# Performance work log

Hardware: AMD Instinct MI355X
Metric: run time of the kernel (lower is better)

The kernel has to match this reference:

```python
import jax, jax.numpy as jnp
import numpy as np

N_HEAD = 8
HIDDENS = 512
NEG_INF = -1e9


def setup_inputs() -> dict:
    key = jax.random.key(0)
    ks = jax.random.split(key, 10)
    B, L, KVP, QP, H, W = 8, 1024, 512, 512, 32, 32
    s = 0.02  # init scale
    return {
        "v": jax.random.normal(ks[0], (B, L, KVP), jnp.float32),
        "k": jax.random.normal(ks[1], (B, L, KVP), jnp.float32),
        "q": jax.random.normal(ks[2], (B, QP, H, W), jnp.float32),
        "mask": jax.random.randint(ks[3], (B, 1, 1, L), 0, 2) > 0,
        "Wv": jax.random.normal(ks[4], (HIDDENS, KVP), jnp.float32) * s,
        "bv": jnp.zeros((HIDDENS,), jnp.float32),
        "Wk": jax.random.normal(ks[5], (HIDDENS, KVP), jnp.float32) * s,
        "bk": jnp.zeros((HIDDENS,), jnp.float32),
        "Wq": jax.random.normal(ks[6], (HIDDENS, QP), jnp.float32) * s,
        "bq": jnp.zeros((HIDDENS,), jnp.float32),
        "Wm": jax.random.normal(ks[7], (512, HIDDENS), jnp.float32) * s,
        "bm": jnp.zeros((512,), jnp.float32),
    }


def reference(v, k, q, mask, Wv, bv, Wk, bk, Wq, bq, Wm, bm):
    B, _, H, W = q.shape
    nh, dh = N_HEAD, HIDDENS // N_HEAD
    # k/v linear projections -> [B, nh, L, dh]
    vh = (v @ Wv.T + bv).reshape(B, -1, nh, dh).transpose(0, 2, 1, 3)
    kh = (k @ Wk.T + bk).reshape(B, -1, nh, dh).transpose(0, 2, 1, 3)
    # q 1x1 conv projection -> [B, hiddens, H, W] -> [B, nh, HW, dh]
    qp = jnp.einsum('bchw,oc->bohw', q, Wq) + bq[None, :, None, None]
    qh = qp.reshape(B, nh, dh, H * W).transpose(0, 1, 3, 2)
    # attention: scores fully materialized [B, nh, HW, L]
    scores = jnp.einsum('bnqd,bnkd->bnqk', qh, kh) / jnp.sqrt(jnp.float32(dh))
    scores = jnp.where(mask, NEG_INF, scores)
    att = jax.nn.softmax(scores, axis=-1)  # dropout omitted (eval mode)
    out = jnp.einsum('bnqk,bnkd->bnqd', att, vh)
    # [B, nh, HW, dh] -> [B, hiddens, H, W]
    out = out.transpose(0, 1, 3, 2).reshape(B, HIDDENS, H, W)
    out = jnp.einsum('bchw,oc->bohw', out, Wm) + bm[None, :, None, None]
    return jax.nn.relu(out)
```

## Files before the change

kernel.cpp:

```cpp
#include <hip/hip_runtime.h>

typedef __attribute__((ext_vector_type(8))) __bf16 bf16x8;
typedef __attribute__((ext_vector_type(4))) float  f32x4;

#define SCALE_Q 0.1803368801111204f

__device__ __forceinline__ unsigned short f2bf(float f) {
    unsigned int u = __builtin_bit_cast(unsigned int, f);
    u += 0x7fffu + ((u >> 16) & 1u);
    return (unsigned short)(u >> 16);
}
__device__ __forceinline__ unsigned int pack2(float a, float b) {
    return (unsigned int)f2bf(a) | ((unsigned int)f2bf(b) << 16);
}

__device__ __forceinline__ int idxW(int row, int ch) {
    return row * 512 + (((ch & ~7) | ((ch ^ row) & 7)) << 3);
}
__device__ __forceinline__ int swz8(int row, int chunk) {
    return row * 64 + ((chunk ^ (row & 7)) << 3);
}
__device__ __forceinline__ bf16x8 fragld(const unsigned short* lds, int row, int kk, int lane) {
    return *(const bf16x8*)(lds + swz8(row, kk * 4 + (lane >> 4)));
}

__global__ __launch_bounds__(256) void ck_w(const float* __restrict__ Wv, const float* __restrict__ Wk,
                                            const float* __restrict__ Wq, const float* __restrict__ Wm,
                                            unsigned short* __restrict__ Wp) {
    int tid = threadIdx.x, lane = tid & 63;
    int gw = blockIdx.x * 4 + (tid >> 6);
    int w = gw >> 9, rem = gw & 511;
    int nb = rem >> 4, kb = rem & 15;
    const float* src = (w == 0) ? Wv : (w == 1) ? Wk : (w == 2) ? Wq : Wm;
    const float* gp = src + (size_t)(nb * 16 + (lane & 15)) * 512 + kb * 32 + (lane >> 4) * 8;
    float4 v0 = *(const float4*)gp, v1 = *(const float4*)(gp + 4);
    uint4 o;
    o.x = pack2(v0.x, v0.y); o.y = pack2(v0.z, v0.w);
    o.z = pack2(v1.x, v1.y); o.w = pack2(v1.z, v1.w);
    *(uint4*)(Wp + ((size_t)w << 18) + ((size_t)((nb * 16 + kb) * 64 + lane)) * 8) = o;
}

__global__ __launch_bounds__(256, 2) void g_proj(const float* __restrict__ kin,
                                                 const float* __restrict__ vin,
                                                 const float* __restrict__ qin,
                                                 const unsigned short* __restrict__ Wp,
                                                 const float* __restrict__ bk,
                                                 const float* __restrict__ bv,
                                                 const float* __restrict__ bq,
                                                 unsigned short* __restrict__ kh,
                                                 unsigned short* __restrict__ vh,
                                                 unsigned short* __restrict__ qh) {
    __shared__ alignas(16) unsigned short As[64 * 512];
    int tid = threadIdx.x, lane = tid & 63, wv = tid >> 6;
    int pid = blockIdx.x;
    int srcSel = (pid < 128) ? 0 : (pid < 256) ? 1 : 2;

    if (srcSel < 2) {
        int panel = (srcSel == 0) ? pid : pid - 128;
        const float* src = ((srcSel == 0) ? kin : vin) + (size_t)panel * 64 * 512;
#pragma unroll
        for (int it = 0; it < 16; ++it) {
            int id = it * 256 + tid, row = id >> 6, ch = id & 63;
            const float* gp = src + (size_t)row * 512 + ch * 8;
            float4 a0 = *(const float4*)gp, a1 = *(const float4*)(gp + 4);
            uint4 w;
            w.x = pack2(a0.x, a0.y); w.y = pack2(a0.z, a0.w);
            w.z = pack2(a1.x, a1.y); w.w = pack2(a1.z, a1.w);
            *(uint4*)(&As[idxW(row, ch)]) = w;
        }
    } else {
        int qi = pid - 256, b = qi >> 4, pp = qi & 15;
        const float* src = qin + (size_t)b * 512 * 1024 + pp * 64;
#pragma unroll
        for (int cc = 0; cc < 8; ++cc) {
            int c0 = cc * 64 + (tid >> 4) * 4;
            int pl = (tid & 15) * 4;
            float rr[4][4];
#pragma unroll
            for (int i = 0; i < 4; ++i) {
                float4 t4 = *(const float4*)(src + (size_t)(c0 + i) * 1024 + pl);
                rr[i][0] = t4.x; rr[i][1] = t4.y; rr[i][2] = t4.z; rr[i][3] = t4.w;
            }
#pragma unroll
            for (int j = 0; j < 4; ++j) {
                int row = pl + j, chunk = c0 >> 3, off = c0 & 7;
                uint2 w2;
                w2.x = pack2(rr[0][j], rr[1][j]);
                w2.y = pack2(rr[2][j], rr[3][j]);
                *(uint2*)(&As[row * 512 + (((chunk & ~7) | ((chunk ^ row) & 7)) << 3) + off]) = w2;
            }
        }
    }
    __syncthreads();

    int wsel = (srcSel == 0) ? 1 : (srcSel == 1) ? 0 : 2;
    const unsigned short* Wb = Wp + ((size_t)wsel << 18);
    f32x4 acc[4][8] = {};
#pragma unroll 2
    for (int kb = 0; kb < 16; ++kb) {
        bf16x8 af[4], bf8[8];
#pragma unroll
        for (int j = 0; j < 8; ++j)
            bf8[j] = *(const bf16x8*)(Wb + ((size_t)(((wv * 8 + j) * 16 + kb) * 64 + lane)) * 8);
#pragma unroll
        for (int i = 0; i < 4; ++i)
            af[i] = *(const bf16x8*)(&As[idxW(i * 16 + (lane & 15), kb * 4 + (lane >> 4))]);
#pragma unroll
        for (int j = 0; j < 8; ++j)
#pragma unroll
            for (int i = 0; i < 4; ++i)
                acc[i][j] = __builtin_amdgcn_mfma_f32_16x16x32_bf16(af[i], bf8[j], acc[i][j], 0, 0, 0);
    }

    if (srcSel < 2) {
        int panel = (srcSel == 0) ? pid : pid - 128;
        unsigned short* dst = (srcSel == 0) ? kh : vh;
        const float* bias = (srcSel == 0) ? bk : bv;
#pragma unroll
        for (int j = 0; j < 8; ++j) {
            int o = wv * 128 + j * 16 + (lane & 15);
            float bb = bias[o];
            int n = o >> 6, d = o & 63;
#pragma unroll
            for (int i = 0; i < 4; ++i)
#pragma unroll
                for (int reg = 0; reg < 4; ++reg) {
                    int r = panel * 64 + i * 16 + ((lane >> 4) << 2) + reg;
                    dst[(((size_t)((r >> 10) * 8 + n)) * 1024 + (r & 1023)) * 64 + d] =
                        f2bf(acc[i][j][reg] + bb);
                }
        }
    } else {
        int qi = pid - 256, b = qi >> 4, pp = qi & 15;
#pragma unroll
        for (int j = 0; j < 8; ++j) {
            int o = wv * 128 + j * 16 + (lane & 15);
            float bb = bq[o];
            int n = o >> 6, d = o & 63;
#pragma unroll
            for (int i = 0; i < 4; ++i)
#pragma unroll
                for (int reg = 0; reg < 4; ++reg) {
                    int p = pp * 64 + i * 16 + ((lane >> 4) << 2) + reg;
                    qh[(((size_t)(b * 8 + n)) * 1024 + p) * 64 + d] =
                        f2bf((acc[i][j][reg] + bb) * SCALE_Q);
                }
        }
    }
}

__global__ __launch_bounds__(256) void k_attn(unsigned short* qa,
                                              const unsigned short* __restrict__ kh,
                                              const unsigned short* __restrict__ vh,
                                              const int* __restrict__ mask) {
    __shared__ alignas(16) unsigned short Qs[64 * 64];
    __shared__ alignas(16) unsigned short Ks[64 * 64];
    __shared__ alignas(16) unsigned short Vs[64 * 64];
    int tid = threadIdx.x, lane = tid & 63, wv = tid >> 6;
    int bn = blockIdx.x;
    int b = bn >> 3;
    int p0 = blockIdx.y * 64;
    const unsigned short* kbase = kh + ((size_t)bn) * 1024 * 64;
    const unsigned short* vbase = vh + ((size_t)bn) * 1024 * 64;
    const int* mbase = mask + (size_t)b * 1024;

    {
        const unsigned short* g = qa + (((size_t)bn) * 1024 + p0) * 64;
#pragma unroll
        for (int s = 0; s < 2; ++s) {
            int idx = tid + s * 256, row = idx >> 3, c = idx & 7;
            *(uint4*)(&Qs[swz8(row, c)]) = *(const uint4*)(g + (size_t)row * 64 + c * 8);
        }
    }
    __syncthreads();
    bf16x8 aq0 = fragld(Qs, wv * 16 + (lane & 15), 0, lane);
    bf16x8 aq1 = fragld(Qs, wv * 16 + (lane & 15), 1, lane);
    unsigned short* Pw = &Qs[wv * 16 * 64];

    int krow = tid >> 3, kch = tid & 7;
    int vtk = (tid >> 4) * 4, vtn = (tid & 15) * 4;
    uint4 kreg[2];
    ushort4 vreg[4];
    int mcur[4];
#pragma unroll
    for (int s = 0; s < 2; ++s)
        kreg[s] = *(const uint4*)(kbase + (size_t)(krow + s * 32) * 64 + kch * 8);
#pragma unroll
    for (int i = 0; i < 4; ++i)
        vreg[i] = *(const ushort4*)(vbase + (size_t)(vtk + i) * 64 + vtn);
#pragma unroll
    for (int j = 0; j < 4; ++j) mcur[j] = mbase[j * 16 + (lane & 15)];

    float mrow[4], lrow[4];
    f32x4 o4[4] = {};
#pragma unroll
    for (int r = 0; r < 4; ++r) { mrow[r] = -3e38f; lrow[r] = 0.f; }

    for (int t = 0; t < 16; ++t) {
        __syncthreads();
#pragma unroll
        for (int s = 0; s < 2; ++s)
            *(uint4*)(&Ks[swz8(krow + s * 32, kch)]) = kreg[s];
#pragma unroll
        for (int j = 0; j < 4; ++j) {
            int row = vtn + j;
            ushort4 w4;
            w4.x = vreg[0][j]; w4.y = vreg[1][j]; w4.z = vreg[2][j]; w4.w = vreg[3][j];
            *(ushort4*)(&Vs[row * 64 + (((vtk >> 3) ^ (row & 7)) << 3) + (vtk & 7)]) = w4;
        }
        __syncthreads();
        if (t < 15) {
            int l1 = (t + 1) * 64;
#pragma unroll
            for (int s = 0; s < 2; ++s)
                kreg[s] = *(const uint4*)(kbase + (size_t)(l1 + krow + s * 32) * 64 + kch * 8);
#pragma unroll
            for (int i = 0; i < 4; ++i)
                vreg[i] = *(const ushort4*)(vbase + (size_t)(l1 + vtk + i) * 64 + vtn);
        }

        f32x4 s[4] = {};
#pragma unroll
        for (int j = 0; j < 4; ++j) {
            bf16x8 bk0 = fragld(Ks, j * 16 + (lane & 15), 0, lane);
            bf16x8 bk1 = fragld(Ks, j * 16 + (lane & 15), 1, lane);
            s[j] = __builtin_amdgcn_mfma_f32_16x16x32_bf16(aq0, bk0, s[j], 0, 0, 0);
            s[j] = __builtin_amdgcn_mfma_f32_16x16x32_bf16(aq1, bk1, s[j], 0, 0, 0);
        }
#pragma unroll
        for (int j = 0; j < 4; ++j) {
            if (mcur[j] != 0) {
#pragma unroll
                for (int reg = 0; reg < 4; ++reg) s[j][reg] = -1e9f;
            }
        }
        if (t < 15) {
            int l1 = (t + 1) * 64;
#pragma unroll
            for (int j = 0; j < 4; ++j) mcur[j] = mbase[l1 + j * 16 + (lane & 15)];
        }

        float pvv[4][4], corr[4];
#pragma unroll
        for (int reg = 0; reg < 4; ++reg) {
            float mx = fmaxf(fmaxf(s[0][reg], s[1][reg]), fmaxf(s[2][reg], s[3][reg]));
#pragma unroll
            for (int off = 1; off < 16; off <<= 1) mx = fmaxf(mx, __shfl_xor(mx, off, 64));
            float mnew = fmaxf(mrow[reg], mx);
            corr[reg] = exp2f(mrow[reg] - mnew);
            mrow[reg] = mnew;
            float sum = 0.f;
#pragma unroll
            for (int j = 0; j < 4; ++j) {
                float p = exp2f(s[j][reg] - mnew);
                pvv[j][reg] = p; sum += p;
            }
#pragma unroll
            for (int off = 1; off < 16; off <<= 1) sum += __shfl_xor(sum, off, 64);
            lrow[reg] = lrow[reg] * corr[reg] + sum;
        }
#pragma unroll
        for (int j = 0; j < 4; ++j) {
            int c = j * 16 + (lane & 15);
#pragma unroll
            for (int reg = 0; reg < 4; ++reg) {
                int pr = ((lane >> 4) << 2) + reg;
                Pw[pr * 64 + (((c >> 3) ^ (pr & 7)) << 3) + (c & 7)] = f2bf(pvv[j][reg]);
            }
        }
#pragma unroll
        for (int jd = 0; jd < 4; ++jd)
#pragma unroll
            for (int reg = 0; reg < 4; ++reg) o4[jd][reg] *= corr[reg];
#pragma unroll
        for (int kk = 0; kk < 2; ++kk) {
            bf16x8 ap = fragld(Pw, (lane & 15), kk, lane);
#pragma unroll
            for (int jd = 0; jd < 4; ++jd) {
                bf16x8 bvf = fragld(Vs, jd * 16 + (lane & 15), kk, lane);
                o4[jd] = __builtin_amdgcn_mfma_f32_16x16x32_bf16(ap, bvf, o4[jd], 0, 0, 0);
            }
        }
    }
    float inv[4];
#pragma unroll
    for (int reg = 0; reg < 4; ++reg) inv[reg] = 1.f / lrow[reg];
    unsigned short* Ow = Pw;
#pragma unroll
    for (int jd = 0; jd < 4; ++jd) {
        int d = jd * 16 + (lane & 15);
        int ch = d >> 3, doff = d & 7;
#pragma unroll
        for (int reg = 0; reg < 4; ++reg) {
            int pr = ((lane >> 4) << 2) + reg;
            Ow[pr * 64 + ((ch ^ (pr & 7)) << 3) + doff] = f2bf(o4[jd][reg] * inv[reg]);
        }
    }
    size_t base = ((size_t)bn * 16 + blockIdx.y) * 4096;
#pragma unroll
    for (int h = 0; h < 2; ++h) {
        int p = lane & 15;
        int ch = h * 4 + (lane >> 4);
        uint4 w = *(const uint4*)(&Ow[p * 64 + ((ch ^ (p & 7)) << 3)]);
        *(uint4*)(qa + base + (size_t)(wv * 2 + h) * 512 + (size_t)lane * 8) = w;
    }
}

__global__ __launch_bounds__(256, 2) void g_final(const unsigned short* __restrict__ aP,
                                                  const unsigned short* __restrict__ Wm8,
                                                  const float* __restrict__ bm,
                                                  float* __restrict__ out) {
    int tid = threadIdx.x, lane = tid & 63, wv = tid >> 6;
    int wr = wv >> 1, wc = wv & 1;
    int b = blockIdx.z, m0 = blockIdx.x * 128, n0 = blockIdx.y * 128;
    int onb = m0 / 16 + wr * 4;
    int pnb = n0 / 16 + wc * 4;
    f32x4 acc[4][4] = {};
#pragma unroll 2
    for (int kb = 0; kb < 16; ++kb) {
        int nh = kb >> 1, h = kb & 1, bn = b * 8 + nh;
        bf16x8 af[4], bf8[4];
#pragma unroll
        for (int i = 0; i < 4; ++i)
            af[i] = *(const bf16x8*)(Wm8 + ((size_t)(((onb + i) * 16 + kb) * 64 + lane)) * 8);
#pragma unroll
        for (int j = 0; j < 4; ++j) {
            int pb = pnb + j;
            bf8[j] = *(const bf16x8*)(aP + ((size_t)bn * 16 + (pb >> 2)) * 4096 +
                                      (size_t)((pb & 3) * 2 + h) * 512 + (size_t)lane * 8);
        }
#pragma unroll
        for (int i = 0; i < 4; ++i)
#pragma unroll
            for (int j = 0; j < 4; ++j)
                acc[i][j] = __builtin_amdgcn_mfma_f32_16x16x32_bf16(af[i], bf8[j], acc[i][j], 0, 0, 0);
    }
#pragma unroll
    for (int i = 0; i < 4; ++i)
#pragma unroll
        for (int reg = 0; reg < 4; ++reg) {
            int o = m0 + wr * 64 + i * 16 + ((lane >> 4) << 2) + reg;
            float bb = bm[o];
#pragma unroll
            for (int j = 0; j < 4; ++j) {
                int p = n0 + wc * 64 + j * 16 + (lane & 15);
                out[((size_t)(b * 512 + o)) * 1024 + p] = fmaxf(acc[i][j][reg] + bb, 0.f);
            }
        }
}

extern "C" void kernel_launch(void* const* d_in, const int* in_sizes, int n_in,
                              void* d_out, int out_size, void* d_ws, size_t ws_size,
                              hipStream_t stream) {
    const float* v  = (const float*)d_in[0];
    const float* k  = (const float*)d_in[1];
    const float* q  = (const float*)d_in[2];
    const int*   mask = (const int*)d_in[3];
    const float* Wv = (const float*)d_in[4];
    const float* bv = (const float*)d_in[5];
    const float* Wk = (const float*)d_in[6];
    const float* bk = (const float*)d_in[7];
    const float* Wq = (const float*)d_in[8];
    const float* bq = (const float*)d_in[9];
    const float* Wm = (const float*)d_in[10];
    const float* bm = (const float*)d_in[11];
    float* out = (float*)d_out;

    const size_t E = (size_t)8 * 8 * 1024 * 64;
    unsigned short* kh = (unsigned short*)d_ws;
    unsigned short* vh = kh + E;
    unsigned short* qh = vh + E;
    unsigned short* Wp = qh + E;

    dim3 blk(256);
    ck_w  <<<512, blk, 0, stream>>>(Wv, Wk, Wq, Wm, Wp);
    g_proj<<<384, blk, 0, stream>>>(k, v, q, Wp, bk, bv, bq, kh, vh, qh);
    k_attn<<<dim3(64, 16), blk, 0, stream>>>(qh, kh, vh, mask);
    g_final<<<dim3(4, 8, 8), blk, 0, stream>>>(qh, Wp + 3 * 262144, bm, out);
}
```

Before: 224.4 us.

## Double-buffer attention K/V via direct global-to-LDS loads with pre-swizzled layouts

The projection kernel now writes K and Q already XOR-swizzled, with stores coalesced through an LDS round-trip. It writes V transposed (d-major) and pre-swizzled. The attention kernel can therefore stream K and V tiles into double-buffered LDS with global_load_lds, instead of staging them in registers and transposing V in shared memory. This cuts VGPR staging, the in-kernel V transpose and one barrier per iteration, and overlaps the next tile's load with compute. In exchange it doubles K/V LDS use, and correctness depends on the global swizzle matching the LDS read pattern exactly.

Measured after the change: 215.0 us. 1.04x faster.

```diff
diff --git a/kernel.cpp b/kernel.cpp
--- a/kernel.cpp
+++ b/kernel.cpp
@@ -22,6 +22,18 @@
 }
 __device__ __forceinline__ bf16x8 fragld(const unsigned short* lds, int row, int kk, int lane) {
     return *(const bf16x8*)(lds + swz8(row, kk * 4 + (lane >> 4)));
+}
+
+__device__ __forceinline__ void gload16(const unsigned short* g, unsigned short* l) {
+    __builtin_amdgcn_global_load_lds((const __attribute__((address_space(1))) void*)g,
+                                     (__attribute__((address_space(3))) void*)l, 16, 0, 0);
+}
+__device__ __forceinline__ void stage16(const unsigned short* g, int ldg,
+                                        unsigned short* lds, int lane, int wv) {
+    const unsigned short* gp = g + (size_t)(wv * 16 + (lane >> 3)) * ldg + (lane & 7) * 8;
+#pragma unroll
+    for (int i = 0; i < 2; ++i)
+        gload16(gp + (size_t)(i * 8) * ldg, lds + (wv * 16 + i * 8) * 64);
 }
 
 __global__ __launch_bounds__(256) void ck_w(const float* __restrict__ Wv, const float* __restrict__ Wk,
@@ -48,7 +60,7 @@
                                                  const float* __restrict__ bv,
                                                  const float* __restrict__ bq,
                                                  unsigned short* __restrict__ kh,
-                                                 unsigned short* __restrict__ vh,
+                                                 unsigned short* __restrict__ vhT,
                                                  unsigned short* __restrict__ qh) {
     __shared__ alignas(16) unsigned short As[64 * 512];
     int tid = threadIdx.x, lane = tid & 63, wv = tid >> 6;
@@ -112,134 +124,113 @@
                 acc[i][j] = __builtin_amdgcn_mfma_f32_16x16x32_bf16(af[i], bf8[j], acc[i][j], 0, 0, 0);
     }
 
-    if (srcSel < 2) {
-        int panel = (srcSel == 0) ? pid : pid - 128;
-        unsigned short* dst = (srcSel == 0) ? kh : vh;
-        const float* bias = (srcSel == 0) ? bk : bv;
+    if (srcSel == 1) {
+        int panel = pid - 128, b = panel >> 4;
+        int win = (panel & 15) * 64;
+#pragma unroll
+        for (int j = 0; j < 8; ++j) {
+            int o = wv * 128 + j * 16 + (lane & 15);
+            float bb = bv[o];
+            int n = o >> 6, d = o & 63;
+            size_t bnbase = ((size_t)(b * 8 + n)) * 65536 + (size_t)d * 1024 + win;
+#pragma unroll
+            for (int i = 0; i < 4; ++i) {
+                int l0 = i * 16 + ((lane >> 4) << 2);
+                uint2 w2;
+                w2.x = pack2(acc[i][j][0] + bb, acc[i][j][1] + bb);
+                w2.y = pack2(acc[i][j][2] + bb, acc[i][j][3] + bb);
+                int off = (((l0 >> 3) ^ (d & 7)) << 3) + (l0 & 7);
+                *(uint2*)(&vhT[bnbase + off]) = w2;
+            }
+        }
+    } else {
+        const float* bias = (srcSel == 0) ? bk : bq;
+        float scl = (srcSel == 0) ? 1.f : SCALE_Q;
+        __syncthreads();
 #pragma unroll
         for (int j = 0; j < 8; ++j) {
             int o = wv * 128 + j * 16 + (lane & 15);
             float bb = bias[o];
-            int n = o >> 6, d = o & 63;
+            int Cd = o >> 3, ob = o & 7;
 #pragma unroll
             for (int i = 0; i < 4; ++i)
 #pragma unroll
                 for (int reg = 0; reg < 4; ++reg) {
-                    int r = panel * 64 + i * 16 + ((lane >> 4) << 2) + reg;
-                    dst[(((size_t)((r >> 10) * 8 + n)) * 1024 + (r & 1023)) * 64 + d] =
-                        f2bf(acc[i][j][reg] + bb);
+                    int l = i * 16 + ((lane >> 4) << 2) + reg;
+                    int Cs = (Cd & ~7) | ((Cd ^ l) & 7);
+                    As[l * 512 + Cs * 8 + ob] = f2bf((acc[i][j][reg] + bb) * scl);
                 }
         }
-    } else {
-        int qi = pid - 256, b = qi >> 4, pp = qi & 15;
-#pragma unroll
-        for (int j = 0; j < 8; ++j) {
-            int o = wv * 128 + j * 16 + (lane & 15);
-            float bb = bq[o];
-            int n = o >> 6, d = o & 63;
-#pragma unroll
-            for (int i = 0; i < 4; ++i)
-#pragma unroll
-                for (int reg = 0; reg < 4; ++reg) {
-                    int p = pp * 64 + i * 16 + ((lane >> 4) << 2) + reg;
-                    qh[(((size_t)(b * 8 + n)) * 1024 + p) * 64 + d] =
-                        f2bf((acc[i][j][reg] + bb) * SCALE_Q);
-                }
+        __syncthreads();
+        unsigned short* dst;
+        int b, rbase;
+        if (srcSel == 0) { b = pid >> 4; rbase = (pid & 15) * 64; dst = kh; }
+        else { int qi = pid - 256; b = qi >> 4; rbase = (qi & 15) * 64; dst = qh; }
+#pragma unroll
+        for (int e = 0; e < 16; ++e) {
+            int n = e >> 1, l = (e & 1) * 32 + (tid >> 3), ch = tid & 7;
+            uint4 w = *(const uint4*)(&As[l * 512 + (n * 8 + ch) * 8]);
+            *(uint4*)(&dst[(((size_t)(b * 8 + n)) * 1024 + rbase + l) * 64 + ch * 8]) = w;
         }
     }
 }
 
 __global__ __launch_bounds__(256) void k_attn(unsigned short* qa,
                                               const unsigned short* __restrict__ kh,
-                                              const unsigned short* __restrict__ vh,
+                                              const unsigned short* __restrict__ vhT,
                                               const int* __restrict__ mask) {
     __shared__ alignas(16) unsigned short Qs[64 * 64];
-    __shared__ alignas(16) unsigned short Ks[64 * 64];
-    __shared__ alignas(16) unsigned short Vs[64 * 64];
+    __shared__ alignas(16) unsigned short Ks[2][64 * 64];
+    __shared__ alignas(16) unsigned short Vs[2][64 * 64];
     int tid = threadIdx.x, lane = tid & 63, wv = tid >> 6;
     int bn = blockIdx.x;
     int b = bn >> 3;
     int p0 = blockIdx.y * 64;
-    const unsigned short* kbase = kh + ((size_t)bn) * 1024 * 64;
-    const unsigned short* vbase = vh + ((size_t)bn) * 1024 * 64;
+    const unsigned short* kbase = kh + ((size_t)bn) * 65536;
+    const unsigned short* vbase = vhT + ((size_t)bn) * 65536;
     const int* mbase = mask + (size_t)b * 1024;
 
-    {
-        const unsigned short* g = qa + (((size_t)bn) * 1024 + p0) * 64;
-#pragma unroll
-        for (int s = 0; s < 2; ++s) {
-            int idx = tid + s * 256, row = idx >> 3, c = idx & 7;
-            *(uint4*)(&Qs[swz8(row, c)]) = *(const uint4*)(g + (size_t)row * 64 + c * 8);
-        }
-    }
+    stage16(qa + (((size_t)bn) * 1024 + p0) * 64, 64, Qs, lane, wv);
+    stage16(kbase, 64, Ks[0], lane, wv);
+    stage16(vbase, 1024, Vs[0], lane, wv);
     __syncthreads();
     bf16x8 aq0 = fragld(Qs, wv * 16 + (lane & 15), 0, lane);
     bf16x8 aq1 = fragld(Qs, wv * 16 + (lane & 15), 1, lane);
     unsigned short* Pw = &Qs[wv * 16 * 64];
 
-    int krow = tid >> 3, kch = tid & 7;
-    int vtk = (tid >> 4) * 4, vtn = (tid & 15) * 4;
-    uint4 kreg[2];
-    ushort4 vreg[4];
-    int mcur[4];
-#pragma unroll
-    for (int s = 0; s < 2; ++s)
-        kreg[s] = *(const uint4*)(kbase + (size_t)(krow + s * 32) * 64 + kch * 8);
-#pragma unroll
-    for (int i = 0; i < 4; ++i)
-        vreg[i] = *(const ushort4*)(vbase + (size_t)(vtk + i) * 64 + vtn);
-#pragma unroll
-    for (int j = 0; j < 4; ++j) mcur[j] = mbase[j * 16 + (lane & 15)];
-
     float mrow[4], lrow[4];
     f32x4 o4[4] = {};
 #pragma unroll
     for (int r = 0; r < 4; ++r) { mrow[r] = -3e38f; lrow[r] = 0.f; }
 
+#pragma unroll 2
     for (int t = 0; t < 16; ++t) {
-        __syncthreads();
-#pragma unroll
-        for (int s = 0; s < 2; ++s)
-            *(uint4*)(&Ks[swz8(krow + s * 32, kch)]) = kreg[s];
-#pragma unroll
-        for (int j = 0; j < 4; ++j) {
-            int row = vtn + j;
-            ushort4 w4;
-            w4.x = vreg[0][j]; w4.y = vreg[1][j]; w4.z = vreg[2][j]; w4.w = vreg[3][j];
-            *(ushort4*)(&Vs[row * 64 + (((vtk >> 3) ^ (row & 7)) << 3) + (vtk & 7)]) = w4;
-        }
-        __syncthreads();
+        int cur = t & 1;
         if (t < 15) {
             int l1 = (t + 1) * 64;
-#pragma unroll
-            for (int s = 0; s < 2; ++s)
-                kreg[s] = *(const uint4*)(kbase + (size_t)(l1 + krow + s * 32) * 64 + kch * 8);
-#pragma unroll
-            for (int i = 0; i < 4; ++i)
-                vreg[i] = *(const ushort4*)(vbase + (size_t)(l1 + vtk + i) * 64 + vtn);
-        }
+            stage16(kbase + (size_t)l1 * 64, 64, Ks[cur ^ 1], lane, wv);
+            stage16(vbase + l1, 1024, Vs[cur ^ 1], lane, wv);
+        }
+        int l0 = t * 64;
+        int mc[4];
+#pragma unroll
+        for (int j = 0; j < 4; ++j) mc[j] = mbase[l0 + j * 16 + (lane & 15)];
 
         f32x4 s[4] = {};
 #pragma unroll
         for (int j = 0; j < 4; ++j) {
-            bf16x8 bk0 = fragld(Ks, j * 16 + (lane & 15), 0, lane);
-            bf16x8 bk1 = fragld(Ks, j * 16 + (lane & 15), 1, lane);
+            bf16x8 bk0 = fragld(Ks[cur], j * 16 + (lane & 15), 0, lane);
+            bf16x8 bk1 = fragld(Ks[cur], j * 16 + (lane & 15), 1, lane);
             s[j] = __builtin_amdgcn_mfma_f32_16x16x32_bf16(aq0, bk0, s[j], 0, 0, 0);
             s[j] = __builtin_amdgcn_mfma_f32_16x16x32_bf16(aq1, bk1, s[j], 0, 0, 0);
         }
 #pragma unroll
         for (int j = 0; j < 4; ++j) {
-            if (mcur[j] != 0) {
+            if (mc[j] != 0) {
 #pragma unroll
                 for (int reg = 0; reg < 4; ++reg) s[j][reg] = -1e9f;
             }
         }
-        if (t < 15) {
-            int l1 = (t + 1) * 64;
-#pragma unroll
-            for (int j = 0; j < 4; ++j) mcur[j] = mbase[l1 + j * 16 + (lane & 15)];
-        }
-
         float pvv[4][4], corr[4];
 #pragma unroll
         for (int reg = 0; reg < 4; ++reg) {
@@ -277,10 +268,11 @@
             bf16x8 ap = fragld(Pw, (lane & 15), kk, lane);
 #pragma unroll
             for (int jd = 0; jd < 4; ++jd) {
-                bf16x8 bvf = fragld(Vs, jd * 16 + (lane & 15), kk, lane);
+                bf16x8 bvf = fragld(Vs[cur], jd * 16 + (lane & 15), kk, lane);
                 o4[jd] = __builtin_amdgcn_mfma_f32_16x16x32_bf16(ap, bvf, o4[jd], 0, 0, 0);
             }
         }
+        __syncthreads();
     }
     float inv[4];
 #pragma unroll
@@ -367,14 +359,14 @@
     float* out = (float*)d_out;
 
     const size_t E = (size_t)8 * 8 * 1024 * 64;
-    unsigned short* kh = (unsigned short*)d_ws;
-    unsigned short* vh = kh + E;
-    unsigned short* qh = vh + E;
-    unsigned short* Wp = qh + E;
+    unsigned short* kh  = (unsigned short*)d_ws;
+    unsigned short* vhT = kh + E;
+    unsigned short* qh  = vhT + E;
+    unsigned short* Wp  = qh + E;
 
     dim3 blk(256);
     ck_w  <<<512, blk, 0, stream>>>(Wv, Wk, Wq, Wm, Wp);
-    g_proj<<<384, blk, 0, stream>>>(k, v, q, Wp, bk, bv, bq, kh, vh, qh);
-    k_attn<<<dim3(64, 16), blk, 0, stream>>>(qh, kh, vh, mask);
+    g_proj<<<384, blk, 0, stream>>>(k, v, q, Wp, bk, bv, bq, kh, vhT, qh);
+    k_attn<<<dim3(64, 16), blk, 0, stream>>>(qh, kh, vhT, mask);
     g_final<<<dim3(4, 8, 8), blk, 0, stream>>>(qh, Wp + 3 * 262144, bm, out);
 }
```
